# Performance work log

Measured on AMD Instinct MI355X. Metric: run time of the kernel, lower is better.

The kernel has to match this reference:

```python
import jax, jax.numpy as jnp
import numpy as np

ALPHA = 1.702
LIMIT = 7.0
TOP_K = 2
B, S, H, E, I = 2, 1024, 768, 8, 768


def setup_inputs() -> dict:
    key = jax.random.key(0)
    ks = jax.random.split(key, 7)
    scale = 0.02
    return {
        "hidden_states": jax.random.normal(ks[0], (B, S, H), dtype=jnp.float32),
        "Wr": jax.random.normal(ks[1], (H, E), dtype=jnp.float32) * scale,
        "br": jax.random.normal(ks[2], (E,), dtype=jnp.float32) * scale,
        "Wgu": jax.random.normal(ks[3], (E, H, 2 * I), dtype=jnp.float32) * scale,
        "bgu": jax.random.normal(ks[4], (E, 2 * I), dtype=jnp.float32) * scale,
        "Wd": jax.random.normal(ks[5], (E, I, H), dtype=jnp.float32) * scale,
        "bd": jax.random.normal(ks[6], (E, H), dtype=jnp.float32) * scale,
    }


def reference(hidden_states, Wr, br, Wgu, bgu, Wd, bd):
    # Router: top-K experts per token, softmax over the K selected logits
    logits = jnp.einsum("bsh,he->bse", hidden_states, Wr) + br
    topk_vals, topk_idx = jax.lax.top_k(logits, TOP_K)        # [B,S,K]
    router_scores = jax.nn.softmax(topk_vals, axis=-1)         # [B,S,K]

    # Dense-over-experts grouped GEMM (sparse_matmul reference: unselected
    # experts are computed but never read by the combine gather below).
    gu = jnp.einsum("bsh,ehf->bsef", hidden_states, Wgu) + bgu  # [B,S,E,2I]
    gu = jnp.minimum(gu, LIMIT)
    gate = gu[..., :I]
    up = jnp.maximum(gu[..., I:], -LIMIT)
    glu = gate * jax.nn.sigmoid(gate * ALPHA)
    activated = (up + 1.0) * glu                                # [B,S,E,I]

    down = jnp.einsum("bsei,eih->bseh", activated, Wd) + bd     # [B,S,E,H]

    # all_to_all_combine (num_devices=1): gather this token's K expert outputs
    sel = jnp.take_along_axis(down, topk_idx[..., None], axis=2)  # [B,S,K,H]
    output = jnp.sum(sel * router_scores[..., None], axis=2)      # [B,S,H]
    return output
```

## Files before the change

kernel.cpp:

```cpp
#include <hip/hip_runtime.h>
#include <hip/hip_bf16.h>
#include <cmath>

#define ALPHA 1.702f
#define LIMIT 7.0f

constexpr int B = 2, S = 1024, H = 768, E = 8, I = 768;
constexpr int T = B * S;
constexpr int TWO_I = 2 * I;
constexpr int CAP = T;
constexpr int NROWS = T * 2;

typedef __attribute__((ext_vector_type(8))) short short8;
typedef __attribute__((ext_vector_type(4))) float floatx4;

__device__ __forceinline__ unsigned short f2bf(float v) {
  __hip_bfloat16 h = __float2bfloat16(v);
  return *reinterpret_cast<unsigned short*>(&h);
}

__device__ __forceinline__ void g2l16(const void* g, void* l) {
  __builtin_amdgcn_global_load_lds(
      (const __attribute__((address_space(1))) void*)g,
      (__attribute__((address_space(3))) void*)l, 16, 0, 0);
}

__global__ __launch_bounds__(64) void router_kernel(
    const float* __restrict__ x, const float* __restrict__ Wr,
    const float* __restrict__ br, int* __restrict__ topk_idx,
    float* __restrict__ topk_w, unsigned short* __restrict__ xb,
    float* __restrict__ out) {
  int t = blockIdx.x;
  int lane = threadIdx.x;
  const float* xr = x + (size_t)t * H;

  float4 z4 = {0.f, 0.f, 0.f, 0.f};
#pragma unroll
  for (int j = 0; j < 3; j++)
    *(float4*)(out + (size_t)t * H + (size_t)(j * 64 + lane) * 4) = z4;

  float acc[E];
#pragma unroll
  for (int e = 0; e < E; e++) acc[e] = 0.0f;

#pragma unroll
  for (int it = 0; it < 3; it++) {
    int h4 = it * 64 + lane;
    float4 xv = *(const float4*)(xr + (size_t)h4 * 4);
    ushort4 xo;
    xo.x = f2bf(xv.x);
    xo.y = f2bf(xv.y);
    xo.z = f2bf(xv.z);
    xo.w = f2bf(xv.w);
    *(ushort4*)(xb + (size_t)t * H + (size_t)h4 * 4) = xo;
    const float* wrow = Wr + (size_t)h4 * 4 * E;
    float xs[4] = {xv.x, xv.y, xv.z, xv.w};
#pragma unroll
    for (int j = 0; j < 4; j++)
#pragma unroll
      for (int e = 0; e < E; e++) acc[e] += xs[j] * wrow[j * E + e];
  }
#pragma unroll
  for (int e = 0; e < E; e++) {
    float v = acc[e];
    for (int off = 32; off > 0; off >>= 1) v += __shfl_down(v, off, 64);
    acc[e] = v;
  }
  if (lane == 0) {
    float logits[E];
#pragma unroll
    for (int e = 0; e < E; e++) logits[e] = acc[e] + br[e];
    int i0 = 0;
    float v0 = logits[0];
#pragma unroll
    for (int e = 1; e < E; e++)
      if (logits[e] > v0) { v0 = logits[e]; i0 = e; }
    int i1 = -1;
    float v1 = -INFINITY;
#pragma unroll
    for (int e = 0; e < E; e++) {
      if (e == i0) continue;
      if (logits[e] > v1) { v1 = logits[e]; i1 = e; }
    }
    float s1 = __expf(v1 - v0);
    float denom = 1.0f + s1;
    topk_idx[t * 2 + 0] = i0;
    topk_idx[t * 2 + 1] = i1;
    topk_w[t * 2 + 0] = 1.0f / denom;
    topk_w[t * 2 + 1] = s1 / denom;
  }
}

__global__ __launch_bounds__(256) void transpose_all(
    const float* __restrict__ Wgu, const float* __restrict__ Wd,
    unsigned short* __restrict__ Wgt, unsigned short* __restrict__ Wdt,
    const int* __restrict__ topk_idx, const float* __restrict__ topk_w,
    int* __restrict__ e_cnt, int* __restrict__ row_token,
    float* __restrict__ row_w) {
  int z = blockIdx.z;
  int tid = threadIdx.x;

  if (z == 16) {
    if (blockIdx.x != 0 || blockIdx.y != 0) return;
    __shared__ int cur[E];
    if (tid < E) cur[tid] = 0;
    __syncthreads();
    for (int i = tid; i < NROWS; i += 256) {
      int e = topk_idx[i];
      int pos = atomicAdd(&cur[e], 1);
      row_token[e * CAP + pos] = i >> 1;
      row_w[e * CAP + pos] = topk_w[i];
    }
    __syncthreads();
    if (tid < E) e_cnt[tid] = cur[tid];
    return;
  }

  int which = z >> 3, e = z & 7;
  int N = which ? H : TWO_I;
  if (which && blockIdx.x >= (H / 64)) return;
  const float* in = which ? (Wd + (size_t)e * H * I)
                          : (Wgu + (size_t)e * H * TWO_I);
  unsigned short* out = which ? (Wdt + (size_t)e * H * I)
                              : (Wgt + (size_t)e * H * TWO_I);
  constexpr int K = 768;
  int n0 = blockIdx.x * 64, k0 = blockIdx.y * 64;

  __shared__ float tile[64][65];
  int jr = tid & 15, r0 = tid >> 4;
#pragma unroll
  for (int p = 0; p < 4; p++) {
    int k = r0 + p * 16;
    float4 v = *(const float4*)(in + (size_t)(k0 + k) * N + n0 + jr * 4);
    tile[k][jr * 4 + 0] = v.x;
    tile[k][jr * 4 + 1] = v.y;
    tile[k][jr * 4 + 2] = v.z;
    tile[k][jr * 4 + 3] = v.w;
  }
  __syncthreads();
#pragma unroll
  for (int p = 0; p < 4; p++) {
    int n = r0 + p * 16;
    ushort4 o;
    o.x = f2bf(tile[jr * 4 + 0][n]);
    o.y = f2bf(tile[jr * 4 + 1][n]);
    o.z = f2bf(tile[jr * 4 + 2][n]);
    o.w = f2bf(tile[jr * 4 + 3][n]);
    *(ushort4*)(out + (size_t)(n0 + n) * K + k0 + jr * 4) = o;
  }
}

__global__ __launch_bounds__(256) void gemm_gu_mfma(
    const unsigned short* __restrict__ xb, const unsigned short* __restrict__ Wgt,
    const float* __restrict__ bgu, const int* __restrict__ e_cnt,
    const int* __restrict__ row_token, unsigned short* __restrict__ act) {
  int e = blockIdx.z;
  int cnt = e_cnt[e];
  int m0 = blockIdx.y * 128;
  if (m0 >= cnt) return;
  int n0 = blockIdx.x * 64;
  int start = e * CAP;
  const unsigned short* Wg = Wgt + (size_t)e * TWO_I * H;
  const float* bias = bgu + (size_t)e * TWO_I;

  __shared__ short As[128 * 64];
  __shared__ short Bg[64 * 64];
  __shared__ short Bu[64 * 64];
  __shared__ int tok[128];

  int tid = threadIdx.x;
  if (tid < 128) {
    int m = m0 + tid;
    tok[tid] = row_token[start + ((m < cnt) ? m : (cnt - 1))];
  }
  __syncthreads();

  int lane = tid & 63;
  int wave = tid >> 6;
  int quad = lane >> 4;
  int lrow = lane & 15;
  int wm = (wave >> 1) * 64;
  int wn = (wave & 1) * 32;

  const unsigned short* gA[4];
  short* lA[4];
#pragma unroll
  for (int r = 0; r < 4; r++) {
    int s = (wave * 4 + r) * 64 + lane;
    int row = s >> 3;
    int g = (s & 7) ^ (row & 7);
    gA[r] = xb + (size_t)tok[row] * H + g * 8;
    lA[r] = &As[(wave * 4 + r) * 64 * 8];
  }
  const unsigned short *gBg[2], *gBu[2];
  short *lBg[2], *lBu[2];
#pragma unroll
  for (int r = 0; r < 2; r++) {
    int s = (wave * 2 + r) * 64 + lane;
    int row = s >> 3;
    int g = (s & 7) ^ (row & 7);
    gBg[r] = Wg + (size_t)(n0 + row) * H + g * 8;
    gBu[r] = gBg[r] + (size_t)I * H;
    lBg[r] = &Bg[(wave * 2 + r) * 64 * 8];
    lBu[r] = &Bu[(wave * 2 + r) * 64 * 8];
  }

  floatx4 accg[4][2], accu[4][2];
#pragma unroll
  for (int i = 0; i < 4; i++)
#pragma unroll
    for (int j = 0; j < 2; j++) {
      accg[i][j] = floatx4{0.f, 0.f, 0.f, 0.f};
      accu[i][j] = floatx4{0.f, 0.f, 0.f, 0.f};
    }

  for (int k0 = 0; k0 < H; k0 += 64) {
#pragma unroll
    for (int r = 0; r < 4; r++) g2l16(gA[r] + k0, lA[r]);
#pragma unroll
    for (int r = 0; r < 2; r++) {
      g2l16(gBg[r] + k0, lBg[r]);
      g2l16(gBu[r] + k0, lBu[r]);
    }
    __syncthreads();

#pragma unroll
    for (int ks = 0; ks < 2; ks++) {
      int c = ks * 4 + quad;
      short8 a[4], bg[2], bu[2];
#pragma unroll
      for (int ti = 0; ti < 4; ti++) {
        int r = wm + ti * 16 + lrow;
        a[ti] = *(const short8*)(&As[(r * 8 + (c ^ (r & 7))) * 8]);
      }
#pragma unroll
      for (int tj = 0; tj < 2; tj++) {
        int r = wn + tj * 16 + lrow;
        bg[tj] = *(const short8*)(&Bg[(r * 8 + (c ^ (r & 7))) * 8]);
        bu[tj] = *(const short8*)(&Bu[(r * 8 + (c ^ (r & 7))) * 8]);
      }
#pragma unroll
      for (int ti = 0; ti < 4; ti++)
#pragma unroll
        for (int tj = 0; tj < 2; tj++) {
          accg[ti][tj] = __builtin_amdgcn_mfma_f32_16x16x32_bf16(
              a[ti], bg[tj], accg[ti][tj], 0, 0, 0);
          accu[ti][tj] = __builtin_amdgcn_mfma_f32_16x16x32_bf16(
              a[ti], bu[tj], accu[ti][tj], 0, 0, 0);
        }
    }
    __syncthreads();
  }

#pragma unroll
  for (int ti = 0; ti < 4; ti++) {
#pragma unroll
    for (int tj = 0; tj < 2; tj++) {
      int ncol = n0 + wn + tj * 16 + lrow;
      float bgv = bias[ncol];
      float buv = bias[I + ncol];
#pragma unroll
      for (int r = 0; r < 4; r++) {
        int m = m0 + wm + ti * 16 + quad * 4 + r;
        if (m < cnt) {
          float g = accg[ti][tj][r] + bgv;
          float u = accu[ti][tj][r] + buv;
          g = fminf(g, LIMIT);
          u = fmaxf(fminf(u, LIMIT), -LIMIT);
          float glu = g / (1.0f + __expf(-ALPHA * g));
          act[(size_t)(start + m) * I + ncol] = f2bf((u + 1.0f) * glu);
        }
      }
    }
  }
}

__global__ __launch_bounds__(256) void gemm_down_mfma(
    const unsigned short* __restrict__ act, const unsigned short* __restrict__ Wdt,
    const float* __restrict__ bd, const int* __restrict__ e_cnt,
    const int* __restrict__ row_token, const float* __restrict__ row_w,
    float* __restrict__ out) {
  int e = blockIdx.z;
  int cnt = e_cnt[e];
  int m0 = blockIdx.y * 128;
  if (m0 >= cnt) return;
  int n0 = blockIdx.x * 64;
  int start = e * CAP;
  const unsigned short* Wd = Wdt + (size_t)e * H * I;
  const float* bias = bd + (size_t)e * H;

  __shared__ short As[128 * 64];
  __shared__ short Bs[64 * 64];
  __shared__ int tok[128];
  __shared__ float wts[128];

  int tid = threadIdx.x;
  if (tid < 128) {
    int m = m0 + tid;
    int mm = (m < cnt) ? m : (cnt - 1);
    tok[tid] = row_token[start + mm];
    wts[tid] = row_w[start + mm];
  }
  __syncthreads();

  int lane = tid & 63;
  int wave = tid >> 6;
  int quad = lane >> 4;
  int lrow = lane & 15;
  int wm = (wave >> 1) * 64;
  int wn = (wave & 1) * 32;

  const unsigned short* gA[4];
  short* lA[4];
#pragma unroll
  for (int r = 0; r < 4; r++) {
    int s = (wave * 4 + r) * 64 + lane;
    int row = s >> 3;
    int g = (s & 7) ^ (row & 7);
    int gm = m0 + row;
    int mm = (gm < cnt) ? gm : (cnt - 1);
    gA[r] = act + (size_t)(start + mm) * I + g * 8;
    lA[r] = &As[(wave * 4 + r) * 64 * 8];
  }
  const unsigned short* gB[2];
  short* lB[2];
#pragma unroll
  for (int r = 0; r < 2; r++) {
    int s = (wave * 2 + r) * 64 + lane;
    int row = s >> 3;
    int g = (s & 7) ^ (row & 7);
    gB[r] = Wd + (size_t)(n0 + row) * I + g * 8;
    lB[r] = &Bs[(wave * 2 + r) * 64 * 8];
  }

  floatx4 acc[4][2];
#pragma unroll
  for (int i = 0; i < 4; i++)
#pragma unroll
    for (int j = 0; j < 2; j++) acc[i][j] = floatx4{0.f, 0.f, 0.f, 0.f};

  for (int k0 = 0; k0 < I; k0 += 64) {
#pragma unroll
    for (int r = 0; r < 4; r++) g2l16(gA[r] + k0, lA[r]);
#pragma unroll
    for (int r = 0; r < 2; r++) g2l16(gB[r] + k0, lB[r]);
    __syncthreads();

#pragma unroll
    for (int ks = 0; ks < 2; ks++) {
      int c = ks * 4 + quad;
      short8 a[4], b[2];
#pragma unroll
      for (int ti = 0; ti < 4; ti++) {
        int r = wm + ti * 16 + lrow;
        a[ti] = *(const short8*)(&As[(r * 8 + (c ^ (r & 7))) * 8]);
      }
#pragma unroll
      for (int tj = 0; tj < 2; tj++) {
        int r = wn + tj * 16 + lrow;
        b[tj] = *(const short8*)(&Bs[(r * 8 + (c ^ (r & 7))) * 8]);
      }
#pragma unroll
      for (int ti = 0; ti < 4; ti++)
#pragma unroll
        for (int tj = 0; tj < 2; tj++)
          acc[ti][tj] = __builtin_amdgcn_mfma_f32_16x16x32_bf16(
              a[ti], b[tj], acc[ti][tj], 0, 0, 0);
    }
    __syncthreads();
  }

#pragma unroll
  for (int ti = 0; ti < 4; ti++) {
#pragma unroll
    for (int tj = 0; tj < 2; tj++) {
      int ncol = n0 + wn + tj * 16 + lrow;
      float bdv = bias[ncol];
#pragma unroll
      for (int r = 0; r < 4; r++) {
        int ml = wm + ti * 16 + quad * 4 + r;
        int m = m0 + ml;
        if (m < cnt) {
          atomicAdd(&out[(size_t)tok[ml] * H + ncol],
                    wts[ml] * (acc[ti][tj][r] + bdv));
        }
      }
    }
  }
}

extern "C" void kernel_launch(void* const* d_in, const int* in_sizes, int n_in,
                              void* d_out, int out_size, void* d_ws,
                              size_t ws_size, hipStream_t stream) {
  const float* x   = (const float*)d_in[0];
  const float* Wr  = (const float*)d_in[1];
  const float* br  = (const float*)d_in[2];
  const float* Wgu = (const float*)d_in[3];
  const float* bgu = (const float*)d_in[4];
  const float* Wd  = (const float*)d_in[5];
  const float* bd  = (const float*)d_in[6];
  float* out = (float*)d_out;

  char* w = (char*)d_ws;
  int* e_cnt = (int*)w;       w += 16 * sizeof(int);
  int* topk_idx = (int*)w;    w += (size_t)T * 2 * sizeof(int);
  float* topk_w = (float*)w;  w += (size_t)T * 2 * sizeof(float);
  int* row_token = (int*)w;   w += (size_t)E * CAP * sizeof(int);
  float* row_w = (float*)w;   w += (size_t)E * CAP * sizeof(float);
  unsigned short* xb  = (unsigned short*)w; w += (size_t)T * H * 2;
  unsigned short* Wgt = (unsigned short*)w; w += (size_t)E * TWO_I * H * 2;
  unsigned short* Wdt = (unsigned short*)w; w += (size_t)E * H * I * 2;
  unsigned short* act = (unsigned short*)w; w += (size_t)E * CAP * I * 2;

  router_kernel<<<T, 64, 0, stream>>>(x, Wr, br, topk_idx, topk_w, xb, out);
  transpose_all<<<dim3(TWO_I / 64, H / 64, 17), 256, 0, stream>>>(
      Wgu, Wd, Wgt, Wdt, topk_idx, topk_w, e_cnt, row_token, row_w);
  gemm_gu_mfma<<<dim3(I / 64, CAP / 128, E), 256, 0, stream>>>(
      xb, Wgt, bgu, e_cnt, row_token, act);
  gemm_down_mfma<<<dim3(H / 64, CAP / 128, E), 256, 0, stream>>>(
      act, Wdt, bd, e_cnt, row_token, row_w, out);
}
```

Before: 179.2 us.

## Double-buffer LDS tiles in both expert GEMMs to overlap loads with MFMA

```diff
diff --git a/kernel.cpp b/kernel.cpp
--- a/kernel.cpp
+++ b/kernel.cpp
@@ -163,9 +163,9 @@
   const unsigned short* Wg = Wgt + (size_t)e * TWO_I * H;
   const float* bias = bgu + (size_t)e * TWO_I;
 
-  __shared__ short As[128 * 64];
-  __shared__ short Bg[64 * 64];
-  __shared__ short Bu[64 * 64];
+  __shared__ short As[2][128 * 64];
+  __shared__ short Bg[2][64 * 64];
+  __shared__ short Bu[2][64 * 64];
   __shared__ int tok[128];
 
   int tid = threadIdx.x;
@@ -183,17 +183,17 @@
   int wn = (wave & 1) * 32;
 
   const unsigned short* gA[4];
-  short* lA[4];
+  int oA[4];
 #pragma unroll
   for (int r = 0; r < 4; r++) {
     int s = (wave * 4 + r) * 64 + lane;
     int row = s >> 3;
     int g = (s & 7) ^ (row & 7);
     gA[r] = xb + (size_t)tok[row] * H + g * 8;
-    lA[r] = &As[(wave * 4 + r) * 64 * 8];
+    oA[r] = (wave * 4 + r) * 64 * 8;
   }
   const unsigned short *gBg[2], *gBu[2];
-  short *lBg[2], *lBu[2];
+  int oB[2];
 #pragma unroll
   for (int r = 0; r < 2; r++) {
     int s = (wave * 2 + r) * 64 + lane;
@@ -201,8 +201,15 @@
     int g = (s & 7) ^ (row & 7);
     gBg[r] = Wg + (size_t)(n0 + row) * H + g * 8;
     gBu[r] = gBg[r] + (size_t)I * H;
-    lBg[r] = &Bg[(wave * 2 + r) * 64 * 8];
-    lBu[r] = &Bu[(wave * 2 + r) * 64 * 8];
+    oB[r] = (wave * 2 + r) * 64 * 8;
+  }
+
+  float bgv[2], buv[2];
+#pragma unroll
+  for (int tj = 0; tj < 2; tj++) {
+    int ncol = n0 + wn + tj * 16 + lrow;
+    bgv[tj] = bias[ncol];
+    buv[tj] = bias[I + ncol];
   }
 
   floatx4 accg[4][2], accu[4][2];
@@ -214,15 +221,34 @@
       accu[i][j] = floatx4{0.f, 0.f, 0.f, 0.f};
     }
 
-  for (int k0 = 0; k0 < H; k0 += 64) {
-#pragma unroll
-    for (int r = 0; r < 4; r++) g2l16(gA[r] + k0, lA[r]);
-#pragma unroll
-    for (int r = 0; r < 2; r++) {
-      g2l16(gBg[r] + k0, lBg[r]);
-      g2l16(gBu[r] + k0, lBu[r]);
-    }
-    __syncthreads();
+  __syncthreads();
+
+#pragma unroll
+  for (int r = 0; r < 4; r++) g2l16(gA[r], &As[0][oA[r]]);
+#pragma unroll
+  for (int r = 0; r < 2; r++) {
+    g2l16(gBg[r], &Bg[0][oB[r]]);
+    g2l16(gBu[r], &Bu[0][oB[r]]);
+  }
+
+  constexpr int NK = H / 64;
+  for (int i = 0; i < NK; i++) {
+    int cb = i & 1;
+    if (i + 1 < NK) {
+      int nb = cb ^ 1;
+      int k1 = (i + 1) * 64;
+#pragma unroll
+      for (int r = 0; r < 4; r++) g2l16(gA[r] + k1, &As[nb][oA[r]]);
+#pragma unroll
+      for (int r = 0; r < 2; r++) {
+        g2l16(gBg[r] + k1, &Bg[nb][oB[r]]);
+        g2l16(gBu[r] + k1, &Bu[nb][oB[r]]);
+      }
+      asm volatile("s_waitcnt vmcnt(8)" ::: "memory");
+    } else {
+      asm volatile("s_waitcnt vmcnt(0)" ::: "memory");
+    }
+    __builtin_amdgcn_s_barrier();
 
 #pragma unroll
     for (int ks = 0; ks < 2; ks++) {
@@ -231,13 +257,13 @@
 #pragma unroll
       for (int ti = 0; ti < 4; ti++) {
         int r = wm + ti * 16 + lrow;
-        a[ti] = *(const short8*)(&As[(r * 8 + (c ^ (r & 7))) * 8]);
+        a[ti] = *(const short8*)(&As[cb][(r * 8 + (c ^ (r & 7))) * 8]);
       }
 #pragma unroll
       for (int tj = 0; tj < 2; tj++) {
         int r = wn + tj * 16 + lrow;
-        bg[tj] = *(const short8*)(&Bg[(r * 8 + (c ^ (r & 7))) * 8]);
-        bu[tj] = *(const short8*)(&Bu[(r * 8 + (c ^ (r & 7))) * 8]);
+        bg[tj] = *(const short8*)(&Bg[cb][(r * 8 + (c ^ (r & 7))) * 8]);
+        bu[tj] = *(const short8*)(&Bu[cb][(r * 8 + (c ^ (r & 7))) * 8]);
       }
 #pragma unroll
       for (int ti = 0; ti < 4; ti++)
@@ -249,7 +275,7 @@
               a[ti], bu[tj], accu[ti][tj], 0, 0, 0);
         }
     }
-    __syncthreads();
+    __builtin_amdgcn_s_barrier();
   }
 
 #pragma unroll
@@ -257,14 +283,12 @@
 #pragma unroll
     for (int tj = 0; tj < 2; tj++) {
       int ncol = n0 + wn + tj * 16 + lrow;
-      float bgv = bias[ncol];
-      float buv = bias[I + ncol];
 #pragma unroll
       for (int r = 0; r < 4; r++) {
         int m = m0 + wm + ti * 16 + quad * 4 + r;
         if (m < cnt) {
-          float g = accg[ti][tj][r] + bgv;
-          float u = accu[ti][tj][r] + buv;
+          float g = accg[ti][tj][r] + bgv[tj];
+          float u = accu[ti][tj][r] + buv[tj];
           g = fminf(g, LIMIT);
           u = fmaxf(fminf(u, LIMIT), -LIMIT);
           float glu = g / (1.0f + __expf(-ALPHA * g));
@@ -289,8 +313,8 @@
   const unsigned short* Wd = Wdt + (size_t)e * H * I;
   const float* bias = bd + (size_t)e * H;
 
-  __shared__ short As[128 * 64];
-  __shared__ short Bs[64 * 64];
+  __shared__ short As[2][128 * 64];
+  __shared__ short Bs[2][64 * 64];
   __shared__ int tok[128];
   __shared__ float wts[128];
 
@@ -311,7 +335,7 @@
   int wn = (wave & 1) * 32;
 
   const unsigned short* gA[4];
-  short* lA[4];
+  int oA[4];
 #pragma unroll
   for (int r = 0; r < 4; r++) {
     int s = (wave * 4 + r) * 64 + lane;
@@ -320,18 +344,22 @@
     int gm = m0 + row;
     int mm = (gm < cnt) ? gm : (cnt - 1);
     gA[r] = act + (size_t)(start + mm) * I + g * 8;
-    lA[r] = &As[(wave * 4 + r) * 64 * 8];
+    oA[r] = (wave * 4 + r) * 64 * 8;
   }
   const unsigned short* gB[2];
-  short* lB[2];
+  int oB[2];
 #pragma unroll
   for (int r = 0; r < 2; r++) {
     int s = (wave * 2 + r) * 64 + lane;
     int row = s >> 3;
     int g = (s & 7) ^ (row & 7);
     gB[r] = Wd + (size_t)(n0 + row) * I + g * 8;
-    lB[r] = &Bs[(wave * 2 + r) * 64 * 8];
-  }
+    oB[r] = (wave * 2 + r) * 64 * 8;
+  }
+
+  float bdv[2];
+#pragma unroll
+  for (int tj = 0; tj < 2; tj++) bdv[tj] = bias[n0 + wn + tj * 16 + lrow];
 
   floatx4 acc[4][2];
 #pragma unroll
@@ -339,12 +367,28 @@
 #pragma unroll
     for (int j = 0; j < 2; j++) acc[i][j] = floatx4{0.f, 0.f, 0.f, 0.f};
 
-  for (int k0 = 0; k0 < I; k0 += 64) {
-#pragma unroll
-    for (int r = 0; r < 4; r++) g2l16(gA[r] + k0, lA[r]);
-#pragma unroll
-    for (int r = 0; r < 2; r++) g2l16(gB[r] + k0, lB[r]);
-    __syncthreads();
+  __syncthreads();
+
+#pragma unroll
+  for (int r = 0; r < 4; r++) g2l16(gA[r], &As[0][oA[r]]);
+#pragma unroll
+  for (int r = 0; r < 2; r++) g2l16(gB[r], &Bs[0][oB[r]]);
+
+  constexpr int NK = I / 64;
+  for (int i = 0; i < NK; i++) {
+    int cb = i & 1;
+    if (i + 1 < NK) {
+      int nb = cb ^ 1;
+      int k1 = (i + 1) * 64;
+#pragma unroll
+      for (int r = 0; r < 4; r++) g2l16(gA[r] + k1, &As[nb][oA[r]]);
+#pragma unroll
+      for (int r = 0; r < 2; r++) g2l16(gB[r] + k1, &Bs[nb][oB[r]]);
+      asm volatile("s_waitcnt vmcnt(6)" ::: "memory");
+    } else {
+      asm volatile("s_waitcnt vmcnt(0)" ::: "memory");
+    }
+    __builtin_amdgcn_s_barrier();
 
 #pragma unroll
     for (int ks = 0; ks < 2; ks++) {
@@ -353,12 +397,12 @@
 #pragma unroll
       for (int ti = 0; ti < 4; ti++) {
         int r = wm + ti * 16 + lrow;
-        a[ti] = *(const short8*)(&As[(r * 8 + (c ^ (r & 7))) * 8]);
+        a[ti] = *(const short8*)(&As[cb][(r * 8 + (c ^ (r & 7))) * 8]);
       }
 #pragma unroll
       for (int tj = 0; tj < 2; tj++) {
         int r = wn + tj * 16 + lrow;
-        b[tj] = *(const short8*)(&Bs[(r * 8 + (c ^ (r & 7))) * 8]);
+        b[tj] = *(const short8*)(&Bs[cb][(r * 8 + (c ^ (r & 7))) * 8]);
       }
 #pragma unroll
       for (int ti = 0; ti < 4; ti++)
@@ -367,7 +411,7 @@
           acc[ti][tj] = __builtin_amdgcn_mfma_f32_16x16x32_bf16(
               a[ti], b[tj], acc[ti][tj], 0, 0, 0);
     }
-    __syncthreads();
+    __builtin_amdgcn_s_barrier();
   }
 
 #pragma unroll
@@ -375,14 +419,13 @@
 #pragma unroll
     for (int tj = 0; tj < 2; tj++) {
       int ncol = n0 + wn + tj * 16 + lrow;
-      float bdv = bias[ncol];
 #pragma unroll
       for (int r = 0; r < 4; r++) {
         int ml = wm + ti * 16 + quad * 4 + r;
         int m = m0 + ml;
         if (m < cnt) {
           atomicAdd(&out[(size_t)tok[ml] * H + ncol],
-                    wts[ml] * (acc[ti][tj][r] + bdv));
+                    wts[ml] * (acc[ti][tj][r] + bdv[tj]));
         }
       }
     }
```

New measurement: 171.6 us. 4.2% less time.
